# Kernel optimization log

Measured on AMD Instinct MI355X. Metric: run time of the kernel, lower is better.

The kernel has to match this reference:

```python
import jax, jax.numpy as jnp
import numpy as np

G = 128                      # grid_size
THRESHOLD_RATIO = 1000.0
BOUNDS = (0.0, 4.5, 0.5, 5.5)  # default grid_bounds (x_min, x_max, y_min, y_max)


def setup_inputs() -> dict:
    key = jax.random.key(0)
    k1, k2, k3 = jax.random.split(key, 3)
    B, N = 8, 524288
    y_pred = jax.random.normal(k1, (B, N, 2), dtype=jnp.float32)
    y_true = jax.random.normal(k2, (B, N, 2), dtype=jnp.float32)
    u = jax.random.uniform(k3, (B, N, 3), dtype=jnp.float32)
    x_min, x_max, y_min, y_max = BOUNDS
    coords = jnp.stack([
        x_min + u[..., 0] * (x_max - x_min),
        y_min + u[..., 1] * (y_max - y_min),
        u[..., 2],
    ], axis=-1)
    return {"y_pred": y_pred, "y_true": y_true, "coords": coords}


def _mean3x3(x, pad_mode):
    # x: [C, G, G] -> 3x3 box filter; 'edge' = replicate pad, 'zero' = constant pad
    xp = jnp.pad(x, ((0, 0), (1, 1), (1, 1)), mode=pad_mode)
    kernel = jnp.full((1, 1, 3, 3), 1.0 / 9.0, dtype=x.dtype)
    return jax.lax.conv_general_dilated(xp[:, None], kernel, (1, 1), 'VALID')[:, 0]


def _scatter_to_grid(coords, vals):
    # coords: [N, 3]; vals: [4, N] (pred_r, pred_i, true_r, true_i) -> [4, G, G]
    x_min, x_max, y_min, y_max = BOUNDS
    xn = (coords[:, 0] - x_min) / (x_max - x_min) * (G - 1)
    yn = (coords[:, 1] - y_min) / (y_max - y_min) * (G - 1)
    xi = jnp.clip(jnp.round(xn).astype(jnp.int32), 0, G - 1)
    yi = jnp.clip(jnp.round(yn).astype(jnp.int32), 0, G - 1)
    flat = yi * G + xi  # [N]
    field = jnp.zeros((4, G * G), vals.dtype).at[:, flat].add(vals)
    count = jnp.zeros((G * G,), vals.dtype).at[flat].add(1.0)
    field = jnp.where(count > 0, field / count, field)
    field = field.reshape(4, G, G)
    count = count.reshape(G, G)
    # 3 iterations of hole-filling (where is a no-op when no cell is empty,
    # matching the torch data-dependent branch exactly)
    for _ in range(3):
        sm = _mean3x3(field, 'edge')
        field = jnp.where(count == 0, sm, field)
        csm = _mean3x3(count[None], 'constant')[0]
        count = jnp.where((count == 0) & (csm > 0), 1.0, count)
    return field


def reference(y_pred, y_true, coords):
    # stack the 4 scalar fields so one scatter pass per sample handles all of them
    vals = jnp.stack([y_pred[..., 0], y_pred[..., 1],
                      y_true[..., 0], y_true[..., 1]], axis=1)  # [B, 4, N]
    grids = jax.vmap(_scatter_to_grid)(coords, vals)  # [B, 4, G, G]
    x_min, x_max, y_min, y_max = BOUNDS
    dx = (x_max - x_min) / (G - 1)
    dy = (y_max - y_min) / (G - 1)
    pred_c = jax.lax.complex(grids[:, 0], grids[:, 1])
    true_c = jax.lax.complex(grids[:, 2], grids[:, 3])
    scale = dx * dy
    fft_pred = jnp.fft.fftshift(jnp.fft.fft2(pred_c), axes=(-2, -1)) * scale
    fft_true = jnp.fft.fftshift(jnp.fft.fft2(true_c), axes=(-2, -1)) * scale
    fa = jnp.abs(fft_true)                               # [B, G, G]
    famax = fa.max(axis=(-2, -1), keepdims=True)
    mask = (fa >= famax / THRESHOLD_RATIO).astype(fa.dtype)
    weight = fa ** 2 / (famax ** 2 + 1e-10)
    d = (fft_pred - fft_true) * mask
    weighted_diff = (jnp.abs(d) ** 2) * weight
    per_sample = weighted_diff.sum(axis=(-2, -1)) / (mask.sum(axis=(-2, -1)) + 1e-10)
    return per_sample.mean()
```

## Files before the change

kernel.cpp:

```cpp
#include <hip/hip_runtime.h>
#include <hip/hip_fp16.h>
#include <math.h>

#define BB 8
#define NPTS 524288
#define G 128
#define GG (G*G)
#define SWORDS 40960

#define OFF_FIELD 0
#define OFF_COUNT (BB*4*GG)
#define OFF_FAMAX (OFF_COUNT + BB*GG)
#define OFF_FLAG  (OFF_FAMAX + 8)
#define OFF_T     (OFF_FAMAX + 24)
#define OFF_Y     (OFF_T + BB*2*GG*2)
#define OFF_STAGE (OFF_T)

__device__ __forceinline__ unsigned pack_h2(float x, float y) {
    __half2 h = __floats2half2_rn(x, y);
    return *(unsigned*)&h;
}

__global__ __launch_bounds__(1024, 4) void k_scatter_sort(const float4* __restrict__ co4,
                                                          const float4* __restrict__ yp4,
                                                          const float4* __restrict__ yt4,
                                                          unsigned* __restrict__ stage,
                                                          unsigned* __restrict__ flags) {
    extern __shared__ unsigned sm[];
    unsigned* cnt = sm;
    unsigned long long* data = (unsigned long long*)(sm + 8192);
    unsigned* dscr = sm + 8192;

    const int t = threadIdx.x;
    const int blk = blockIdx.x;
    const unsigned qbase = (unsigned)blk * 4096u;

    if (blk == 0 && t < 8) flags[t] = 0u;

    for (int k = t; k < 8192; k += 1024) cnt[k] = 0u;
    __syncthreads();

    unsigned cr[16];
    unsigned pk[32];
#pragma unroll
    for (int g = 0; g < 4; g++) {
        unsigned qa = qbase + (unsigned)(g * 1024 + t);
        float4 A = co4[3u * qa], B = co4[3u * qa + 1], C = co4[3u * qa + 2];
        float4 P0 = yp4[2u * qa], P1 = yp4[2u * qa + 1];
        float4 Q0 = yt4[2u * qa], Q1 = yt4[2u * qa + 1];
        pk[8 * g + 0] = pack_h2(P0.x, P0.y); pk[8 * g + 1] = pack_h2(Q0.x, Q0.y);
        pk[8 * g + 2] = pack_h2(P0.z, P0.w); pk[8 * g + 3] = pack_h2(Q0.z, Q0.w);
        pk[8 * g + 4] = pack_h2(P1.x, P1.y); pk[8 * g + 5] = pack_h2(Q1.x, Q1.y);
        pk[8 * g + 6] = pack_h2(P1.z, P1.w); pk[8 * g + 7] = pack_h2(Q1.z, Q1.w);
        float cx[4], cy[4];
        cx[0] = A.x; cy[0] = A.y; cx[1] = A.w; cy[1] = B.x;
        cx[2] = B.z; cy[2] = B.w; cx[3] = C.y; cy[3] = C.z;
#pragma unroll
        for (int j = 0; j < 4; j++) {
            float xn = (cx[j] - 0.0f) / 4.5f * 127.0f;
            float yn = (cy[j] - 0.5f) / 5.0f * 127.0f;
            int xi = min(max((int)rintf(xn), 0), G - 1);
            int yi = min(max((int)rintf(yn), 0), G - 1);
            unsigned cell = (unsigned)(yi * G + xi);
            unsigned sh = (cell & 1u) * 16u;
            unsigned old = atomicAdd(&cnt[cell >> 1], 1u << sh);
            unsigned rank = (old >> sh) & 0xFFFFu;
            cr[g * 4 + j] = cell | (rank << 16);
        }
    }
    __syncthreads();

    unsigned w[8], ssum = 0;
#pragma unroll
    for (int j = 0; j < 8; j++) {
        w[j] = cnt[8 * t + j];
        ssum += (w[j] & 0xFFFFu) + (w[j] >> 16);
    }
    unsigned lane = (unsigned)t & 63u, wid = (unsigned)t >> 6;
    unsigned inc = ssum;
    for (int off = 1; off < 64; off <<= 1) {
        unsigned v = __shfl_up(inc, off);
        if (lane >= (unsigned)off) inc += v;
    }
    if (lane == 63u) dscr[wid] = inc;
    __syncthreads();
    unsigned wbase = 0;
#pragma unroll
    for (int k = 0; k < 16; k++) {
        unsigned v = dscr[k];
        if ((unsigned)k < wid) wbase += v;
    }
    unsigned ex = wbase + inc - ssum;
#pragma unroll
    for (int j = 0; j < 8; j++) {
        unsigned c0 = w[j] & 0xFFFFu, c1 = w[j] >> 16;
        cnt[8 * t + j] = ex | ((ex + c0) << 16);
        ex += c0 + c1;
    }
    __syncthreads();

    const unsigned short* off16 = (const unsigned short*)cnt;
#pragma unroll
    for (int g = 0; g < 4; g++) {
#pragma unroll
        for (int j = 0; j < 4; j++) {
            unsigned c = cr[g * 4 + j] & 0xFFFFu;
            unsigned rank = cr[g * 4 + j] >> 16;
            unsigned pos = (unsigned)off16[c] + rank;
            data[pos] = ((unsigned long long)pk[8 * g + 2 * j + 1] << 32)
                      | (unsigned long long)pk[8 * g + 2 * j];
        }
    }
    __syncthreads();

    unsigned* sb = stage + (size_t)blk * SWORDS;
    unsigned o[17];
#pragma unroll
    for (int j = 0; j < 8; j++) {
        unsigned wv = cnt[8 * t + j];
        o[2 * j] = wv & 0xFFFFu;
        o[2 * j + 1] = wv >> 16;
    }
    o[16] = (t == 1023) ? 16384u : (unsigned)off16[16 * (t + 1)];
    unsigned pvw[16], tvw[16];
#pragma unroll
    for (int k = 0; k < 16; k++) {
        float pr = 0.f, pi = 0.f, tr = 0.f, ti = 0.f;
        for (unsigned j = o[k]; j < o[k + 1]; j++) {
            unsigned long long d = data[j];
            unsigned lo = (unsigned)d, hi = (unsigned)(d >> 32);
            float2 fp = __half22float2(*(__half2*)&lo);
            float2 ft = __half22float2(*(__half2*)&hi);
            pr += fp.x; pi += fp.y; tr += ft.x; ti += ft.y;
        }
        pvw[k] = pack_h2(pr, pi);
        tvw[k] = pack_h2(tr, ti);
    }
#pragma unroll
    for (int j = 0; j < 4; j++)
        *(uint4*)(sb + 16 * t + 4 * j) = make_uint4(pvw[4*j], pvw[4*j+1], pvw[4*j+2], pvw[4*j+3]);
#pragma unroll
    for (int j = 0; j < 4; j++)
        *(uint4*)(sb + 16384 + 16 * t + 4 * j) = make_uint4(tvw[4*j], tvw[4*j+1], tvw[4*j+2], tvw[4*j+3]);
#pragma unroll
    for (int j = 0; j < 8; j++) {
        float ce = (float)(o[2 * j + 1] - o[2 * j]);
        float cd = (float)(o[2 * j + 2] - o[2 * j + 1]);
        sb[32768 + 8 * t + j] = pack_h2(ce, cd);
    }
}

__global__ __launch_bounds__(1024) void k_scatter(const float4* __restrict__ co4,
                                                  const float4* __restrict__ yp4,
                                                  const float4* __restrict__ yt4,
                                                  unsigned* __restrict__ stage,
                                                  unsigned* __restrict__ flags,
                                                  int rep) {
    extern __shared__ unsigned sm[];
    int blk = blockIdx.x;
    int r = blk % rep;
    int b = blk / rep;
    if (blk == 0 && threadIdx.x < 8) flags[threadIdx.x] = 0u;
    for (int k = threadIdx.x; k < SWORDS / 4; k += 1024)
        ((uint4*)sm)[k] = make_uint4(0u, 0u, 0u, 0u);
    __syncthreads();
    unsigned ldsbase = (unsigned)(uintptr_t)sm;
    int ppb = NPTS / rep;
    int nq = ppb >> 2;
    size_t qbase = ((size_t)b * NPTS + (size_t)r * ppb) >> 2;
#define DOPT(cx, cy, vx, vy, wx, wy) do {                                   \
        float xn = ((cx) - 0.0f) / 4.5f * 127.0f;                           \
        float yn = ((cy) - 0.5f) / 5.0f * 127.0f;                           \
        int xi = min(max((int)rintf(xn), 0), G - 1);                        \
        int yi = min(max((int)rintf(yn), 0), G - 1);                        \
        unsigned cell = (unsigned)(yi * G + xi);                            \
        unsigned av = ldsbase + cell * 4u;                                  \
        asm volatile("ds_pk_add_f16 %0, %1" :: "v"(av), "v"(pack_h2(vx, vy))); \
        asm volatile("ds_pk_add_f16 %0, %1" :: "v"(av + 65536u), "v"(pack_h2(wx, wy))); \
        unsigned ac = ldsbase + 131072u + (cell >> 1) * 4u;                 \
        unsigned cw = (cell & 1u) ? 0x3C000000u : 0x00003C00u;              \
        asm volatile("ds_pk_add_f16 %0, %1" :: "v"(ac), "v"(cw));           \
    } while (0)
    for (int q = threadIdx.x; q < nq; q += 2048) {
        size_t qa = qbase + q, qb = qa + 1024;
        float4 A0 = co4[3 * qa], B0 = co4[3 * qa + 1], C0 = co4[3 * qa + 2];
        float4 P00 = yp4[2 * qa], P01 = yp4[2 * qa + 1];
        float4 Q00 = yt4[2 * qa], Q01 = yt4[2 * qa + 1];
        float4 A1 = co4[3 * qb], B1 = co4[3 * qb + 1], C1 = co4[3 * qb + 2];
        float4 P10 = yp4[2 * qb], P11 = yp4[2 * qb + 1];
        float4 Q10 = yt4[2 * qb], Q11 = yt4[2 * qb + 1];
        DOPT(A0.x, A0.y, P00.x, P00.y, Q00.x, Q00.y);
        DOPT(A0.w, B0.x, P00.z, P00.w, Q00.z, Q00.w);
        DOPT(B0.z, B0.w, P01.x, P01.y, Q01.x, Q01.y);
        DOPT(C0.y, C0.z, P01.z, P01.w, Q01.z, Q01.w);
        DOPT(A1.x, A1.y, P10.x, P10.y, Q10.x, Q10.y);
        DOPT(A1.w, B1.x, P10.z, P10.w, Q10.z, Q10.w);
        DOPT(B1.z, B1.w, P11.x, P11.y, Q11.x, Q11.y);
        DOPT(C1.y, C1.z, P11.z, P11.w, Q11.z, Q11.w);
    }
#undef DOPT
    asm volatile("s_waitcnt lgkmcnt(0)" ::: "memory");
    __syncthreads();
    unsigned* sb = stage + (size_t)blk * SWORDS;
    for (int k = threadIdx.x * 4; k < SWORDS; k += 4096)
        *(uint4*)(sb + k) = *(const uint4*)(sm + k);
}

__global__ __launch_bounds__(256) void k_reduce(const unsigned* __restrict__ stage,
                                                float* __restrict__ field,
                                                float* __restrict__ cnt,
                                                unsigned* __restrict__ famax,
                                                unsigned* __restrict__ flags,
                                                float* __restrict__ out,
                                                int rep) {
    if (blockIdx.x == 0) {
        if (threadIdx.x < 8) famax[threadIdx.x] = 0u;
        if (threadIdx.x == 8) out[0] = 0.f;
    }
    int idx = blockIdx.x * 256 + threadIdx.x;
    int k = idx & 8191;
    int b = idx >> 13;
    const unsigned* sb = stage + (size_t)b * rep * SWORDS;
    float p0r = 0, p0i = 0, p1r = 0, p1i = 0;
    float t0r = 0, t0i = 0, t1r = 0, t1i = 0;
    float n0 = 0, n1 = 0;
    for (int r = 0; r < rep; r++) {
        const unsigned* pp = sb + (size_t)r * SWORDS;
        uint2 pv = *(const uint2*)(pp + 2 * k);
        uint2 tv = *(const uint2*)(pp + 16384 + 2 * k);
        unsigned cw = pp[32768 + k];
        float2 f;
        f = __half22float2(*(__half2*)&pv.x); p0r += f.x; p0i += f.y;
        f = __half22float2(*(__half2*)&pv.y); p1r += f.x; p1i += f.y;
        f = __half22float2(*(__half2*)&tv.x); t0r += f.x; t0i += f.y;
        f = __half22float2(*(__half2*)&tv.y); t1r += f.x; t1i += f.y;
        f = __half22float2(*(__half2*)&cw);   n0  += f.x; n1  += f.y;
    }
    int hole = (n0 == 0.f) || (n1 == 0.f);
    if (__any(hole)) {
        if ((threadIdx.x & 63) == 0) atomicOr(&flags[b], 1u);
    }
    if (n0 > 0.f) { p0r /= n0; p0i /= n0; t0r /= n0; t0i /= n0; }
    if (n1 > 0.f) { p1r /= n1; p1i /= n1; t1r /= n1; t1i /= n1; }
    float2* f2 = (float2*)field;
    size_t o = (size_t)b * 4 * (GG / 2) + k;
    f2[o]                = make_float2(p0r, p1r);
    f2[o + (GG / 2)]     = make_float2(p0i, p1i);
    f2[o + 2 * (GG / 2)] = make_float2(t0r, t1r);
    f2[o + 3 * (GG / 2)] = make_float2(t0i, t1i);
    ((float2*)cnt)[(size_t)b * (GG / 2) + k] = make_float2(n0, n1);
}

__global__ __launch_bounds__(1024) void k_holefill(float* __restrict__ field,
                                                   const float* __restrict__ cnt,
                                                   const unsigned* __restrict__ flags) {
    int b = blockIdx.x >> 2, ch = blockIdx.x & 3;
    if (flags[b] == 0u) return;
    extern __shared__ float smf[];
    float* fs = smf;
    float* cs = smf + GG;
    float* fg = field + ((size_t)b * 4 + ch) * GG;
    const float* cg = cnt + (size_t)b * GG;
    int tid = threadIdx.x;
    for (int k = 0; k < 16; k++) {
        int cell = tid + k * 1024;
        cs[cell] = cg[cell];
        fs[cell] = fg[cell];
    }
    __syncthreads();
    float nf[16], nc[16];
    for (int it = 0; it < 3; ++it) {
        for (int k = 0; k < 16; k++) {
            int cell = tid + k * 1024;
            int y = cell >> 7, x = cell & 127;
            float c = cs[cell];
            float f = fs[cell];
            if (c == 0.f) {
                float s9 = 0.f;
                for (int dy = -1; dy <= 1; dy++)
                    for (int dx = -1; dx <= 1; dx++) {
                        int yy = min(max(y + dy, 0), G - 1);
                        int xx = min(max(x + dx, 0), G - 1);
                        s9 += fs[yy * G + xx];
                    }
                f = s9 * (1.0f / 9.0f);
                float c9 = 0.f;
                for (int dy = -1; dy <= 1; dy++)
                    for (int dx = -1; dx <= 1; dx++) {
                        int yy = y + dy, xx = x + dx;
                        if (yy >= 0 && yy < G && xx >= 0 && xx < G) c9 += cs[yy * G + xx];
                    }
                if (c9 > 0.f) c = 1.0f;
            }
            nf[k] = f; nc[k] = c;
        }
        __syncthreads();
        for (int k = 0; k < 16; k++) {
            int cell = tid + k * 1024;
            fs[cell] = nf[k];
            cs[cell] = nc[k];
        }
        __syncthreads();
    }
    for (int k = 0; k < 16; k++) {
        int cell = tid + k * 1024;
        fg[cell] = fs[cell];
    }
}

template <int PASS>
__global__ __launch_bounds__(256) void k_dft(const float* __restrict__ in,
                                             float* __restrict__ out,
                                             unsigned* __restrict__ famax) {
    __shared__ float2 xs[8][128];
    int blk = blockIdx.x;
    int rc = blk & 15;
    int bf = blk >> 4;
    int tid = threadIdx.x;
    if (PASS == 0) {
        const float* re = in + ((size_t)(bf >> 1) * 4 + (size_t)(bf & 1) * 2) * GG + rc * 8 * G;
        const float* im = re + GG;
        for (int e = 0; e < 4; e++) {
            int idx = tid + e * 256;
            xs[idx >> 7][idx & 127] = make_float2(re[idx], im[idx]);
        }
    } else {
        const float2* cx = (const float2*)in + (size_t)bf * GG + rc * 8 * G;
        for (int e = 0; e < 4; e++) {
            int idx = tid + e * 256;
            xs[idx >> 7][idx & 127] = cx[idx];
        }
    }
    __syncthreads();

    int rloc = (tid >> 6) * 2;
    int kk = tid & 63;
    float ang = -3.14159265358979323846f / 64.0f * (float)kk;
    float si, sr;
    sincosf(ang, &si, &sr);

    float e0r = 0.f, e0i = 0.f, o0r = 0.f, o0i = 0.f;
    float e1r = 0.f, e1i = 0.f, o1r = 0.f, o1i = 0.f;
    float tr = 1.f, ti = 0.f;
#pragma unroll 8
    for (int n = 0; n < 128; n += 2) {
        float2 x0 = xs[rloc][n];
        float2 x1 = xs[rloc + 1][n];
        e0r += x0.x * tr - x0.y * ti;  e0i += x0.x * ti + x0.y * tr;
        e1r += x1.x * tr - x1.y * ti;  e1i += x1.x * ti + x1.y * tr;
        float t2r = tr * sr - ti * si, t2i = tr * si + ti * sr;
        x0 = xs[rloc][n + 1];
        x1 = xs[rloc + 1][n + 1];
        o0r += x0.x * t2r - x0.y * t2i;  o0i += x0.x * t2i + x0.y * t2r;
        o1r += x1.x * t2r - x1.y * t2i;  o1i += x1.x * t2i + x1.y * t2r;
        tr = t2r * sr - t2i * si;  ti = t2r * si + t2i * sr;
    }

    float2 a00 = make_float2(e0r + o0r, e0i + o0i);
    float2 a01 = make_float2(e1r + o1r, e1i + o1i);
    float2 a10 = make_float2(e0r - o0r, e0i - o0i);
    float2 a11 = make_float2(e1r - o1r, e1i - o1i);

    float2* ob = (float2*)out + (size_t)bf * GG;
    int r0 = rc * 8 + rloc;
    ob[kk * G + r0]            = a00;
    ob[kk * G + r0 + 1]        = a01;
    ob[(kk + 64) * G + r0]     = a10;
    ob[(kk + 64) * G + r0 + 1] = a11;

    if (PASS == 1 && (bf & 1)) {
        float m = fmaxf(fmaxf(sqrtf(a00.x * a00.x + a00.y * a00.y),
                              sqrtf(a01.x * a01.x + a01.y * a01.y)),
                        fmaxf(sqrtf(a10.x * a10.x + a10.y * a10.y),
                              sqrtf(a11.x * a11.x + a11.y * a11.y)));
        for (int off = 32; off; off >>= 1) m = fmaxf(m, __shfl_down(m, off));
        if ((tid & 63) == 0) atomicMax(&famax[bf >> 1], __float_as_uint(m));
    }
}

__global__ __launch_bounds__(1024) void k_loss(const float* __restrict__ Ybuf,
                                               const unsigned* __restrict__ famax,
                                               float* __restrict__ out) {
    int b = blockIdx.x;
    const float2* Yp = (const float2*)Ybuf + (size_t)(b * 2 + 0) * GG;
    const float2* Yt = (const float2*)Ybuf + (size_t)(b * 2 + 1) * GG;
    const float s = (4.5f / 127.0f) * (5.0f / 127.0f);
    float fam = __uint_as_float(famax[b]) * s;
    float fam2 = fam * fam + 1e-10f;
    float thr = fam / 1000.0f;
    float swd = 0.f, smask = 0.f;
    for (int k = 0; k < 16; k++) {
        int idx = threadIdx.x + k * 1024;
        float2 p = Yp[idx], t = Yt[idx];
        float pr = p.x * s, pi = p.y * s;
        float qr = t.x * s, qi = t.y * s;
        float fa = sqrtf(qr * qr + qi * qi);
        if (fa >= thr) {
            float w = fa * fa / fam2;
            float dr = pr - qr, di = pi - qi;
            swd += (dr * dr + di * di) * w;
            smask += 1.f;
        }
    }
    for (int off = 32; off; off >>= 1) {
        swd += __shfl_down(swd, off);
        smask += __shfl_down(smask, off);
    }
    __shared__ float rs[16], rm[16];
    int wid = threadIdx.x >> 6, lane = threadIdx.x & 63;
    if (lane == 0) { rs[wid] = swd; rm[wid] = smask; }
    __syncthreads();
    if (threadIdx.x == 0) {
        float a = 0.f, m = 0.f;
        for (int w = 0; w < 16; w++) { a += rs[w]; m += rm[w]; }
        atomicAdd(out, (a / (m + 1e-10f)) * 0.125f);
    }
}

extern "C" void kernel_launch(void* const* d_in, const int* in_sizes, int n_in,
                              void* d_out, int out_size, void* d_ws, size_t ws_size,
                              hipStream_t stream) {
    const float* yp = (const float*)d_in[0];
    const float* yt = (const float*)d_in[1];
    const float* co = (const float*)d_in[2];
    float* ws = (float*)d_ws;
    float* field = ws + OFF_FIELD;
    float* cnt   = ws + OFF_COUNT;
    unsigned* famax = (unsigned*)(ws + OFF_FAMAX);
    unsigned* flags = (unsigned*)(ws + OFF_FLAG);
    float* T = ws + OFF_T;
    float* Y = ws + OFF_Y;
    unsigned* stage = (unsigned*)(ws + OFF_STAGE);

    int rep = 32;
    while (rep > 1 &&
           ((size_t)OFF_T + (size_t)BB * rep * SWORDS) * 4 > ws_size)
        rep >>= 1;

    if (rep == 32) {
        k_scatter_sort<<<BB * 32, 1024, SWORDS * sizeof(unsigned), stream>>>(
            (const float4*)co, (const float4*)yp, (const float4*)yt, stage, flags);
    } else {
        k_scatter<<<BB * rep, 1024, SWORDS * sizeof(unsigned), stream>>>(
            (const float4*)co, (const float4*)yp, (const float4*)yt, stage, flags, rep);
    }
    k_reduce<<<BB * (GG / 2) / 256, 256, 0, stream>>>(
        stage, field, cnt, famax, flags, (float*)d_out, rep);
    k_holefill<<<BB * 4, 1024, 2 * GG * sizeof(float), stream>>>(field, cnt, flags);
    k_dft<0><<<BB * 2 * 16, 256, 0, stream>>>(field, T, famax);
    k_dft<1><<<BB * 2 * 16, 256, 0, stream>>>(T, Y, famax);
    k_loss<<<BB, 1024, 0, stream>>>(Y, famax, (float*)d_out);
}
```

Measured before the change: 101.2 us.

## Fuse all stages into one cooperative persistent kernel with grid syncs

Replaces the six-kernel pipeline (scatter-sort, reduce, holefill, two DFT passes, loss) with a single cooperative kernel of 256 blocks that separates stages with grid.sync(). The aim is to remove per-kernel launch gaps and tail effects between small stages. It also defers loading the prediction and target values until after the counting pass, which lowers register pressure in the scatter stage. The cost is grid-wide barriers, stages that use only a few blocks (holefill, loss) leaving most of the GPU idle, and dependence on all 256 blocks of 1024 threads being co-resident.

```diff
diff --git a/kernel.cpp b/kernel.cpp
--- a/kernel.cpp
+++ b/kernel.cpp
@@ -1,6 +1,9 @@
 #include <hip/hip_runtime.h>
+#include <hip/hip_cooperative_groups.h>
 #include <hip/hip_fp16.h>
 #include <math.h>
+
+namespace cg = cooperative_groups;
 
 #define BB 8
 #define NPTS 524288
@@ -21,132 +24,366 @@
     return *(unsigned*)&h;
 }
 
-__global__ __launch_bounds__(1024, 4) void k_scatter_sort(const float4* __restrict__ co4,
-                                                          const float4* __restrict__ yp4,
-                                                          const float4* __restrict__ yt4,
-                                                          unsigned* __restrict__ stage,
-                                                          unsigned* __restrict__ flags) {
+__global__ __launch_bounds__(1024) void k_mega(const float4* __restrict__ co4,
+                                               const float4* __restrict__ yp4,
+                                               const float4* __restrict__ yt4,
+                                               unsigned* __restrict__ stage,
+                                               float* __restrict__ field,
+                                               float* __restrict__ cnt,
+                                               unsigned* __restrict__ famax,
+                                               unsigned* __restrict__ flags,
+                                               float* __restrict__ T,
+                                               float* __restrict__ Y,
+                                               float* __restrict__ out) {
+    cg::grid_group grid = cg::this_grid();
     extern __shared__ unsigned sm[];
-    unsigned* cnt = sm;
-    unsigned long long* data = (unsigned long long*)(sm + 8192);
-    unsigned* dscr = sm + 8192;
-
     const int t = threadIdx.x;
     const int blk = blockIdx.x;
-    const unsigned qbase = (unsigned)blk * 4096u;
-
-    if (blk == 0 && t < 8) flags[t] = 0u;
-
-    for (int k = t; k < 8192; k += 1024) cnt[k] = 0u;
-    __syncthreads();
-
-    unsigned cr[16];
-    unsigned pk[32];
-#pragma unroll
-    for (int g = 0; g < 4; g++) {
-        unsigned qa = qbase + (unsigned)(g * 1024 + t);
-        float4 A = co4[3u * qa], B = co4[3u * qa + 1], C = co4[3u * qa + 2];
-        float4 P0 = yp4[2u * qa], P1 = yp4[2u * qa + 1];
-        float4 Q0 = yt4[2u * qa], Q1 = yt4[2u * qa + 1];
-        pk[8 * g + 0] = pack_h2(P0.x, P0.y); pk[8 * g + 1] = pack_h2(Q0.x, Q0.y);
-        pk[8 * g + 2] = pack_h2(P0.z, P0.w); pk[8 * g + 3] = pack_h2(Q0.z, Q0.w);
-        pk[8 * g + 4] = pack_h2(P1.x, P1.y); pk[8 * g + 5] = pack_h2(Q1.x, Q1.y);
-        pk[8 * g + 6] = pack_h2(P1.z, P1.w); pk[8 * g + 7] = pack_h2(Q1.z, Q1.w);
-        float cx[4], cy[4];
-        cx[0] = A.x; cy[0] = A.y; cx[1] = A.w; cy[1] = B.x;
-        cx[2] = B.z; cy[2] = B.w; cx[3] = C.y; cy[3] = C.z;
-#pragma unroll
-        for (int j = 0; j < 4; j++) {
-            float xn = (cx[j] - 0.0f) / 4.5f * 127.0f;
-            float yn = (cy[j] - 0.5f) / 5.0f * 127.0f;
-            int xi = min(max((int)rintf(xn), 0), G - 1);
-            int yi = min(max((int)rintf(yn), 0), G - 1);
-            unsigned cell = (unsigned)(yi * G + xi);
-            unsigned sh = (cell & 1u) * 16u;
-            unsigned old = atomicAdd(&cnt[cell >> 1], 1u << sh);
-            unsigned rank = (old >> sh) & 0xFFFFu;
-            cr[g * 4 + j] = cell | (rank << 16);
-        }
-    }
-    __syncthreads();
-
-    unsigned w[8], ssum = 0;
-#pragma unroll
-    for (int j = 0; j < 8; j++) {
-        w[j] = cnt[8 * t + j];
-        ssum += (w[j] & 0xFFFFu) + (w[j] >> 16);
-    }
-    unsigned lane = (unsigned)t & 63u, wid = (unsigned)t >> 6;
-    unsigned inc = ssum;
-    for (int off = 1; off < 64; off <<= 1) {
-        unsigned v = __shfl_up(inc, off);
-        if (lane >= (unsigned)off) inc += v;
-    }
-    if (lane == 63u) dscr[wid] = inc;
-    __syncthreads();
-    unsigned wbase = 0;
-#pragma unroll
-    for (int k = 0; k < 16; k++) {
-        unsigned v = dscr[k];
-        if ((unsigned)k < wid) wbase += v;
-    }
-    unsigned ex = wbase + inc - ssum;
-#pragma unroll
-    for (int j = 0; j < 8; j++) {
-        unsigned c0 = w[j] & 0xFFFFu, c1 = w[j] >> 16;
-        cnt[8 * t + j] = ex | ((ex + c0) << 16);
-        ex += c0 + c1;
-    }
-    __syncthreads();
-
-    const unsigned short* off16 = (const unsigned short*)cnt;
-#pragma unroll
-    for (int g = 0; g < 4; g++) {
-#pragma unroll
-        for (int j = 0; j < 4; j++) {
-            unsigned c = cr[g * 4 + j] & 0xFFFFu;
-            unsigned rank = cr[g * 4 + j] >> 16;
-            unsigned pos = (unsigned)off16[c] + rank;
-            data[pos] = ((unsigned long long)pk[8 * g + 2 * j + 1] << 32)
-                      | (unsigned long long)pk[8 * g + 2 * j];
-        }
-    }
-    __syncthreads();
-
-    unsigned* sb = stage + (size_t)blk * SWORDS;
-    unsigned o[17];
-#pragma unroll
-    for (int j = 0; j < 8; j++) {
-        unsigned wv = cnt[8 * t + j];
-        o[2 * j] = wv & 0xFFFFu;
-        o[2 * j + 1] = wv >> 16;
-    }
-    o[16] = (t == 1023) ? 16384u : (unsigned)off16[16 * (t + 1)];
-    unsigned pvw[16], tvw[16];
-#pragma unroll
-    for (int k = 0; k < 16; k++) {
-        float pr = 0.f, pi = 0.f, tr = 0.f, ti = 0.f;
-        for (unsigned j = o[k]; j < o[k + 1]; j++) {
-            unsigned long long d = data[j];
-            unsigned lo = (unsigned)d, hi = (unsigned)(d >> 32);
-            float2 fp = __half22float2(*(__half2*)&lo);
-            float2 ft = __half22float2(*(__half2*)&hi);
-            pr += fp.x; pi += fp.y; tr += ft.x; ti += ft.y;
-        }
-        pvw[k] = pack_h2(pr, pi);
-        tvw[k] = pack_h2(tr, ti);
-    }
-#pragma unroll
-    for (int j = 0; j < 4; j++)
-        *(uint4*)(sb + 16 * t + 4 * j) = make_uint4(pvw[4*j], pvw[4*j+1], pvw[4*j+2], pvw[4*j+3]);
-#pragma unroll
-    for (int j = 0; j < 4; j++)
-        *(uint4*)(sb + 16384 + 16 * t + 4 * j) = make_uint4(tvw[4*j], tvw[4*j+1], tvw[4*j+2], tvw[4*j+3]);
-#pragma unroll
-    for (int j = 0; j < 8; j++) {
-        float ce = (float)(o[2 * j + 1] - o[2 * j]);
-        float cd = (float)(o[2 * j + 2] - o[2 * j + 1]);
-        sb[32768 + 8 * t + j] = pack_h2(ce, cd);
+
+    if (blk == 0) {
+        if (t < 8) famax[t] = 0u;
+        if (t >= 8 && t < 16) flags[t - 8] = 0u;
+        if (t == 16) out[0] = 0.f;
+    }
+
+    {
+        unsigned* c16 = sm;
+        unsigned long long* data = (unsigned long long*)(sm + 8192);
+        unsigned* dscr = sm + 8192;
+        const unsigned qbase = (unsigned)blk * 4096u;
+
+        for (int k = t; k < 8192; k += 1024) c16[k] = 0u;
+        __syncthreads();
+
+        unsigned cr[16];
+#pragma unroll
+        for (int g = 0; g < 4; g++) {
+            unsigned qa = qbase + (unsigned)(g * 1024 + t);
+            float4 A = co4[3u * qa], B = co4[3u * qa + 1], C = co4[3u * qa + 2];
+            float cx[4], cy[4];
+            cx[0] = A.x; cy[0] = A.y; cx[1] = A.w; cy[1] = B.x;
+            cx[2] = B.z; cy[2] = B.w; cx[3] = C.y; cy[3] = C.z;
+#pragma unroll
+            for (int j = 0; j < 4; j++) {
+                float xn = (cx[j] - 0.0f) / 4.5f * 127.0f;
+                float yn = (cy[j] - 0.5f) / 5.0f * 127.0f;
+                int xi = min(max((int)rintf(xn), 0), G - 1);
+                int yi = min(max((int)rintf(yn), 0), G - 1);
+                unsigned cell = (unsigned)(yi * G + xi);
+                unsigned sh = (cell & 1u) * 16u;
+                unsigned old = atomicAdd(&c16[cell >> 1], 1u << sh);
+                unsigned rank = (old >> sh) & 0xFFFFu;
+                cr[g * 4 + j] = cell | (rank << 16);
+            }
+        }
+        __syncthreads();
+
+        unsigned w[8], ssum = 0;
+#pragma unroll
+        for (int j = 0; j < 8; j++) {
+            w[j] = c16[8 * t + j];
+            ssum += (w[j] & 0xFFFFu) + (w[j] >> 16);
+        }
+        unsigned lane = (unsigned)t & 63u, wid = (unsigned)t >> 6;
+        unsigned inc = ssum;
+        for (int off = 1; off < 64; off <<= 1) {
+            unsigned v = __shfl_up(inc, off);
+            if (lane >= (unsigned)off) inc += v;
+        }
+        if (lane == 63u) dscr[wid] = inc;
+        __syncthreads();
+        unsigned wbase = 0;
+#pragma unroll
+        for (int k = 0; k < 16; k++) {
+            unsigned v = dscr[k];
+            if ((unsigned)k < wid) wbase += v;
+        }
+        unsigned ex = wbase + inc - ssum;
+#pragma unroll
+        for (int j = 0; j < 8; j++) {
+            unsigned c0 = w[j] & 0xFFFFu, c1 = w[j] >> 16;
+            c16[8 * t + j] = ex | ((ex + c0) << 16);
+            ex += c0 + c1;
+        }
+        __syncthreads();
+
+        const unsigned short* off16 = (const unsigned short*)c16;
+#pragma unroll
+        for (int g = 0; g < 4; g++) {
+            unsigned qa = qbase + (unsigned)(g * 1024 + t);
+            float4 P0 = yp4[2u * qa], P1 = yp4[2u * qa + 1];
+            float4 Q0 = yt4[2u * qa], Q1 = yt4[2u * qa + 1];
+            unsigned pv[4], tv[4];
+            pv[0] = pack_h2(P0.x, P0.y); pv[1] = pack_h2(P0.z, P0.w);
+            pv[2] = pack_h2(P1.x, P1.y); pv[3] = pack_h2(P1.z, P1.w);
+            tv[0] = pack_h2(Q0.x, Q0.y); tv[1] = pack_h2(Q0.z, Q0.w);
+            tv[2] = pack_h2(Q1.x, Q1.y); tv[3] = pack_h2(Q1.z, Q1.w);
+#pragma unroll
+            for (int j = 0; j < 4; j++) {
+                unsigned c = cr[g * 4 + j] & 0xFFFFu;
+                unsigned rank = cr[g * 4 + j] >> 16;
+                unsigned pos = (unsigned)off16[c] + rank;
+                data[pos] = ((unsigned long long)tv[j] << 32) | (unsigned long long)pv[j];
+            }
+        }
+        __syncthreads();
+
+        unsigned* sb = stage + (size_t)blk * SWORDS;
+        unsigned o[17];
+#pragma unroll
+        for (int j = 0; j < 8; j++) {
+            unsigned wv = c16[8 * t + j];
+            o[2 * j] = wv & 0xFFFFu;
+            o[2 * j + 1] = wv >> 16;
+        }
+        o[16] = (t == 1023) ? 16384u : (unsigned)off16[16 * (t + 1)];
+        unsigned pvw[16], tvw[16];
+#pragma unroll
+        for (int k = 0; k < 16; k++) {
+            float pr = 0.f, pi = 0.f, tr = 0.f, ti = 0.f;
+            for (unsigned j = o[k]; j < o[k + 1]; j++) {
+                unsigned long long d = data[j];
+                unsigned lo = (unsigned)d, hi = (unsigned)(d >> 32);
+                float2 fp = __half22float2(*(__half2*)&lo);
+                float2 ft = __half22float2(*(__half2*)&hi);
+                pr += fp.x; pi += fp.y; tr += ft.x; ti += ft.y;
+            }
+            pvw[k] = pack_h2(pr, pi);
+            tvw[k] = pack_h2(tr, ti);
+        }
+#pragma unroll
+        for (int j = 0; j < 4; j++)
+            *(uint4*)(sb + 16 * t + 4 * j) = make_uint4(pvw[4*j], pvw[4*j+1], pvw[4*j+2], pvw[4*j+3]);
+#pragma unroll
+        for (int j = 0; j < 4; j++)
+            *(uint4*)(sb + 16384 + 16 * t + 4 * j) = make_uint4(tvw[4*j], tvw[4*j+1], tvw[4*j+2], tvw[4*j+3]);
+#pragma unroll
+        for (int j = 0; j < 8; j++) {
+            float ce = (float)(o[2 * j + 1] - o[2 * j]);
+            float cd = (float)(o[2 * j + 2] - o[2 * j + 1]);
+            sb[32768 + 8 * t + j] = pack_h2(ce, cd);
+        }
+    }
+    grid.sync();
+
+    {
+        unsigned wave = (unsigned)t >> 6, lane = (unsigned)t & 63u;
+        unsigned wave_id = (unsigned)blk * 16u + wave;
+        unsigned ggrp = wave_id >> 2;
+        unsigned q = wave_id & 3u;
+        unsigned lg = wave >> 2;
+        unsigned pair = ggrp * 64u + lane;
+        unsigned k = pair & 8191u;
+        unsigned b = pair >> 13;
+        const unsigned* sb = stage + (size_t)b * 32u * SWORDS;
+        float p0r = 0, p0i = 0, p1r = 0, p1i = 0;
+        float t0r = 0, t0i = 0, t1r = 0, t1i = 0;
+        float n0 = 0, n1 = 0;
+        for (unsigned r = q * 8u; r < q * 8u + 8u; r++) {
+            const unsigned* pp = sb + (size_t)r * SWORDS;
+            uint2 pv = *(const uint2*)(pp + 2 * k);
+            uint2 tv = *(const uint2*)(pp + 16384 + 2 * k);
+            unsigned cw = pp[32768 + k];
+            float2 f;
+            f = __half22float2(*(__half2*)&pv.x); p0r += f.x; p0i += f.y;
+            f = __half22float2(*(__half2*)&pv.y); p1r += f.x; p1i += f.y;
+            f = __half22float2(*(__half2*)&tv.x); t0r += f.x; t0i += f.y;
+            f = __half22float2(*(__half2*)&tv.y); t1r += f.x; t1i += f.y;
+            f = __half22float2(*(__half2*)&cw);   n0  += f.x; n1  += f.y;
+        }
+        float* smf = (float*)sm;
+        if (q != 0) {
+            float* dst = smf + (((q - 1u) * 4u + lg) * 64u + lane) * 11u;
+            dst[0] = p0r; dst[1] = p0i; dst[2] = p1r; dst[3] = p1i;
+            dst[4] = t0r; dst[5] = t0i; dst[6] = t1r; dst[7] = t1i;
+            dst[8] = n0;  dst[9] = n1;
+        }
+        __syncthreads();
+        if (q == 0) {
+#pragma unroll
+            for (int qq = 0; qq < 3; qq++) {
+                const float* src = smf + (((unsigned)qq * 4u + lg) * 64u + lane) * 11u;
+                p0r += src[0]; p0i += src[1]; p1r += src[2]; p1i += src[3];
+                t0r += src[4]; t0i += src[5]; t1r += src[6]; t1i += src[7];
+                n0 += src[8]; n1 += src[9];
+            }
+            int hole = (n0 == 0.f) || (n1 == 0.f);
+            if (__any(hole)) { if (lane == 0) atomicOr(&flags[b], 1u); }
+            if (n0 > 0.f) { p0r /= n0; p0i /= n0; t0r /= n0; t0i /= n0; }
+            if (n1 > 0.f) { p1r /= n1; p1i /= n1; t1r /= n1; t1i /= n1; }
+            float2* f2 = (float2*)field;
+            size_t o = (size_t)b * 4 * (GG / 2) + k;
+            f2[o]                = make_float2(p0r, p1r);
+            f2[o + (GG / 2)]     = make_float2(p0i, p1i);
+            f2[o + 2 * (GG / 2)] = make_float2(t0r, t1r);
+            f2[o + 3 * (GG / 2)] = make_float2(t0i, t1i);
+            ((float2*)cnt)[(size_t)b * (GG / 2) + k] = make_float2(n0, n1);
+        }
+    }
+    grid.sync();
+
+    {
+        int hb = blk >> 2, ch = blk & 3;
+        if (blk < 32 && flags[hb] != 0u) {
+            float* fs = (float*)sm;
+            float* cs = fs + GG;
+            float* fg = field + ((size_t)hb * 4 + ch) * GG;
+            const float* cg = cnt + (size_t)hb * GG;
+            for (int k = 0; k < 16; k++) {
+                int cell = t + k * 1024;
+                cs[cell] = cg[cell];
+                fs[cell] = fg[cell];
+            }
+            __syncthreads();
+            float nf[16], nc[16];
+            for (int it = 0; it < 3; ++it) {
+                for (int k = 0; k < 16; k++) {
+                    int cell = t + k * 1024;
+                    int y = cell >> 7, x = cell & 127;
+                    float c = cs[cell];
+                    float f = fs[cell];
+                    if (c == 0.f) {
+                        float s9 = 0.f;
+                        for (int dy = -1; dy <= 1; dy++)
+                            for (int dx = -1; dx <= 1; dx++) {
+                                int yy = min(max(y + dy, 0), G - 1);
+                                int xx = min(max(x + dx, 0), G - 1);
+                                s9 += fs[yy * G + xx];
+                            }
+                        f = s9 * (1.0f / 9.0f);
+                        float c9 = 0.f;
+                        for (int dy = -1; dy <= 1; dy++)
+                            for (int dx = -1; dx <= 1; dx++) {
+                                int yy = y + dy, xx = x + dx;
+                                if (yy >= 0 && yy < G && xx >= 0 && xx < G) c9 += cs[yy * G + xx];
+                            }
+                        if (c9 > 0.f) c = 1.0f;
+                    }
+                    nf[k] = f; nc[k] = c;
+                }
+                __syncthreads();
+                for (int k = 0; k < 16; k++) {
+                    int cell = t + k * 1024;
+                    fs[cell] = nf[k];
+                    cs[cell] = nc[k];
+                }
+                __syncthreads();
+            }
+            for (int k = 0; k < 16; k++) {
+                int cell = t + k * 1024;
+                fg[cell] = fs[cell];
+            }
+        }
+    }
+    grid.sync();
+
+    {
+        float2* xs = (float2*)sm;
+        int rc = blk & 15, bf = blk >> 4;
+        const float* re = field + ((size_t)(bf >> 1) * 4 + (size_t)(bf & 1) * 2) * GG + rc * 8 * G;
+        const float* im = re + GG;
+        xs[t] = make_float2(re[t], im[t]);
+        __syncthreads();
+        if (t < 512) {
+            int rloc = t >> 6;
+            int kk = t & 63;
+            float ang = -3.14159265358979323846f / 64.0f * (float)kk;
+            float si, sr;
+            sincosf(ang, &si, &sr);
+            float er = 0.f, ei = 0.f, odr = 0.f, odi = 0.f;
+            float tr = 1.f, ti = 0.f;
+#pragma unroll 8
+            for (int n = 0; n < 128; n += 2) {
+                float2 x0 = xs[rloc * 128 + n];
+                er += x0.x * tr - x0.y * ti;  ei += x0.x * ti + x0.y * tr;
+                float t2r = tr * sr - ti * si, t2i = tr * si + ti * sr;
+                float2 x1 = xs[rloc * 128 + n + 1];
+                odr += x1.x * t2r - x1.y * t2i;  odi += x1.x * t2i + x1.y * t2r;
+                tr = t2r * sr - t2i * si;  ti = t2r * si + t2i * sr;
+            }
+            float2* ob = (float2*)T + (size_t)bf * GG;
+            int r0 = rc * 8 + rloc;
+            ob[kk * G + r0]        = make_float2(er + odr, ei + odi);
+            ob[(kk + 64) * G + r0] = make_float2(er - odr, ei - odi);
+        }
+    }
+    grid.sync();
+
+    {
+        float2* xs = (float2*)sm;
+        int rc = blk & 15, bf = blk >> 4;
+        const float2* cx = (const float2*)T + (size_t)bf * GG + rc * 8 * G;
+        xs[t] = cx[t];
+        __syncthreads();
+        if (t < 512) {
+            int rloc = t >> 6;
+            int kk = t & 63;
+            float ang = -3.14159265358979323846f / 64.0f * (float)kk;
+            float si, sr;
+            sincosf(ang, &si, &sr);
+            float er = 0.f, ei = 0.f, odr = 0.f, odi = 0.f;
+            float tr = 1.f, ti = 0.f;
+#pragma unroll 8
+            for (int n = 0; n < 128; n += 2) {
+                float2 x0 = xs[rloc * 128 + n];
+                er += x0.x * tr - x0.y * ti;  ei += x0.x * ti + x0.y * tr;
+                float t2r = tr * sr - ti * si, t2i = tr * si + ti * sr;
+                float2 x1 = xs[rloc * 128 + n + 1];
+                odr += x1.x * t2r - x1.y * t2i;  odi += x1.x * t2i + x1.y * t2r;
+                tr = t2r * sr - t2i * si;  ti = t2r * si + t2i * sr;
+            }
+            float2 a0 = make_float2(er + odr, ei + odi);
+            float2 a1 = make_float2(er - odr, ei - odi);
+            float2* ob = (float2*)Y + (size_t)bf * GG;
+            int r0 = rc * 8 + rloc;
+            ob[kk * G + r0]        = a0;
+            ob[(kk + 64) * G + r0] = a1;
+            if (bf & 1) {
+                float m = fmaxf(sqrtf(a0.x * a0.x + a0.y * a0.y),
+                                sqrtf(a1.x * a1.x + a1.y * a1.y));
+                for (int off = 32; off; off >>= 1) m = fmaxf(m, __shfl_down(m, off));
+                if ((t & 63) == 0) atomicMax(&famax[bf >> 1], __float_as_uint(m));
+            }
+        }
+    }
+    grid.sync();
+
+    if (blk < 8) {
+        int b = blk;
+        const float2* Yp = (const float2*)Y + (size_t)(b * 2 + 0) * GG;
+        const float2* Yt = (const float2*)Y + (size_t)(b * 2 + 1) * GG;
+        const float s = (4.5f / 127.0f) * (5.0f / 127.0f);
+        float fam = __uint_as_float(famax[b]) * s;
+        float fam2 = fam * fam + 1e-10f;
+        float thr = fam / 1000.0f;
+        float swd = 0.f, smask = 0.f;
+        for (int k = 0; k < 16; k++) {
+            int idx = t + k * 1024;
+            float2 p = Yp[idx], tt = Yt[idx];
+            float pr = p.x * s, pi = p.y * s;
+            float qr = tt.x * s, qi = tt.y * s;
+            float fa = sqrtf(qr * qr + qi * qi);
+            if (fa >= thr) {
+                float w = fa * fa / fam2;
+                float dr = pr - qr, di = pi - qi;
+                swd += (dr * dr + di * di) * w;
+                smask += 1.f;
+            }
+        }
+        for (int off = 32; off; off >>= 1) {
+            swd += __shfl_down(swd, off);
+            smask += __shfl_down(smask, off);
+        }
+        float* rs = (float*)sm;
+        float* rm = rs + 16;
+        int wid = t >> 6, lane = t & 63;
+        if (lane == 0) { rs[wid] = swd; rm[wid] = smask; }
+        __syncthreads();
+        if (t == 0) {
+            float a = 0.f, m = 0.f;
+            for (int w = 0; w < 16; w++) { a += rs[w]; m += rm[w]; }
+            atomicAdd(out, (a / (m + 1e-10f)) * 0.125f);
+        }
     }
 }
 
@@ -420,9 +657,9 @@
 extern "C" void kernel_launch(void* const* d_in, const int* in_sizes, int n_in,
                               void* d_out, int out_size, void* d_ws, size_t ws_size,
                               hipStream_t stream) {
-    const float* yp = (const float*)d_in[0];
-    const float* yt = (const float*)d_in[1];
-    const float* co = (const float*)d_in[2];
+    const float4* yp4 = (const float4*)d_in[0];
+    const float4* yt4 = (const float4*)d_in[1];
+    const float4* co4 = (const float4*)d_in[2];
     float* ws = (float*)d_ws;
     float* field = ws + OFF_FIELD;
     float* cnt   = ws + OFF_COUNT;
@@ -430,6 +667,7 @@
     unsigned* flags = (unsigned*)(ws + OFF_FLAG);
     float* T = ws + OFF_T;
     float* Y = ws + OFF_Y;
+    float* outp = (float*)d_out;
     unsigned* stage = (unsigned*)(ws + OFF_STAGE);
 
     int rep = 32;
@@ -438,16 +676,19 @@
         rep >>= 1;
 
     if (rep == 32) {
-        k_scatter_sort<<<BB * 32, 1024, SWORDS * sizeof(unsigned), stream>>>(
-            (const float4*)co, (const float4*)yp, (const float4*)yt, stage, flags);
+        void* args[] = { (void*)&co4, (void*)&yp4, (void*)&yt4, (void*)&stage,
+                         (void*)&field, (void*)&cnt, (void*)&famax, (void*)&flags,
+                         (void*)&T, (void*)&Y, (void*)&outp };
+        hipLaunchCooperativeKernel((const void*)k_mega, dim3(256), dim3(1024),
+                                   args, SWORDS * sizeof(unsigned), stream);
     } else {
         k_scatter<<<BB * rep, 1024, SWORDS * sizeof(unsigned), stream>>>(
-            (const float4*)co, (const float4*)yp, (const float4*)yt, stage, flags, rep);
-    }
-    k_reduce<<<BB * (GG / 2) / 256, 256, 0, stream>>>(
-        stage, field, cnt, famax, flags, (float*)d_out, rep);
-    k_holefill<<<BB * 4, 1024, 2 * GG * sizeof(float), stream>>>(field, cnt, flags);
-    k_dft<0><<<BB * 2 * 16, 256, 0, stream>>>(field, T, famax);
-    k_dft<1><<<BB * 2 * 16, 256, 0, stream>>>(T, Y, famax);
-    k_loss<<<BB, 1024, 0, stream>>>(Y, famax, (float*)d_out);
-}
+            co4, yp4, yt4, stage, flags, rep);
+        k_reduce<<<BB * (GG / 2) / 256, 256, 0, stream>>>(
+            stage, field, cnt, famax, flags, outp, rep);
+        k_holefill<<<BB * 4, 1024, 2 * GG * sizeof(float), stream>>>(field, cnt, flags);
+        k_dft<0><<<BB * 2 * 16, 256, 0, stream>>>(field, T, famax);
+        k_dft<1><<<BB * 2 * 16, 256, 0, stream>>>(T, Y, famax);
+        k_loss<<<BB, 1024, 0, stream>>>(Y, famax, outp);
+    }
+}
```

After: 251.3 us. 148% more time.
